# Kernel optimization log

Hardware: AMD Instinct MI355X
Metric: run time of the kernel (lower is better)

The kernel has to match this reference:

```python
import jax, jax.numpy as jnp
import numpy as np

S, B, D, H, V, MF = 50, 128, 512, 512, 30000, 32
PAD = 0


def setup_inputs() -> dict:
    key = jax.random.key(0)
    ks = jax.random.split(key, 10)
    inp = {
        "user": jax.random.normal(ks[0], (B, MF), dtype=jnp.float32),
        "item": jax.random.normal(ks[1], (B, MF), dtype=jnp.float32),
        "review_input": jax.random.randint(ks[2], (S, B), 0, V, dtype=jnp.int64),
        "review_target": jax.random.randint(ks[3], (S, B), 0, V, dtype=jnp.int64),
        # learned parameters
        "word_emb": jax.random.normal(ks[4], (V, D), dtype=jnp.float32) * 0.02,
        "W_ih": jax.random.normal(ks[5], (3 * H, D), dtype=jnp.float32) * (1.0 / np.sqrt(D)),
        "W_hh": jax.random.normal(ks[6], (3 * H, H), dtype=jnp.float32) * (1.0 / np.sqrt(H)),
        "b_ih": jnp.zeros((3 * H,), dtype=jnp.float32),
        "b_hh": jnp.zeros((3 * H,), dtype=jnp.float32),
        "W_out": jax.random.normal(ks[7], (V, H), dtype=jnp.float32) * (1.0 / np.sqrt(H)),
        "b_out": jnp.zeros((V,), dtype=jnp.float32),
    }
    return inp


def _gru_forward(review_input, word_emb, W_ih, W_hh, b_ih, b_hh, W_out, b_out, batch):
    Hdim = W_hh.shape[1]
    h0 = jnp.zeros((batch, Hdim), dtype=word_emb.dtype)  # encoder returns zeros
    x = word_emb[review_input]  # [S, B, D] embedding lookup (dropout is identity in eval)

    def step(h, x_t):
        gi = x_t @ W_ih.T + b_ih            # [B, 3H]
        gh = h @ W_hh.T + b_hh              # [B, 3H]
        i_r, i_z, i_n = jnp.split(gi, 3, axis=-1)
        h_r, h_z, h_n = jnp.split(gh, 3, axis=-1)
        r = jax.nn.sigmoid(i_r + h_r)
        z = jax.nn.sigmoid(i_z + h_z)
        n = jnp.tanh(i_n + r * h_n)
        h_new = (1.0 - z) * n + z * h
        return h_new, h_new

    _, hs = jax.lax.scan(step, h0, x)       # [S, B, H]
    logits = jnp.einsum('sbh,vh->sbv', hs, W_out) + b_out  # decode from hidden_state
    return logits.reshape(-1, W_out.shape[0])  # [S*B, V], same row order as torch.cat


def reference(user, item, review_input, review_target, word_emb, W_ih, W_hh,
              b_ih, b_hh, W_out, b_out):
    batch = user.shape[0]
    logits = _gru_forward(review_input, word_emb, W_ih, W_hh, b_ih, b_hh,
                          W_out, b_out, batch)
    targets = review_target.reshape(-1)                     # [S*B]
    logp = jax.nn.log_softmax(logits, axis=-1)
    nll = -jnp.take_along_axis(logp, targets[:, None], axis=-1)[:, 0]
    mask = (targets != PAD)
    out_loss = jnp.where(mask, nll, 0.0)                    # reduction='none', ignore_index=PAD
    denom = jnp.maximum(jnp.sum(mask.astype(logits.dtype)), 1.0)
    obj = jnp.sum(out_loss) / denom                         # mean over non-pad tokens
    return (out_loss, obj)
```

## Files before the change

kernel.cpp:

```cpp
#include <hip/hip_runtime.h>
#include <hip/hip_bf16.h>

typedef __attribute__((ext_vector_type(8))) short short8;
typedef __attribute__((ext_vector_type(4))) float floatx4;

#define S_LEN  50
#define BATCH  128
#define DIM    512
#define HID    512
#define G3     1536
#define VOCAB  30000
#define TOKENS 6400
#define NB256  118
#define NVC    472
#define NWG    (25 * NB256)

__device__ __forceinline__ float bf2f(short u) {
    union { unsigned int i; float f; } c;
    c.i = ((unsigned int)(unsigned short)u) << 16;
    return c.f;
}
__device__ __forceinline__ unsigned short f2bf(float x) {
    __hip_bfloat16 h = __float2bfloat16(x);
    unsigned short u;
    __builtin_memcpy(&u, &h, 2);
    return u;
}
__device__ __forceinline__ void gl_lds16(const void* g, void* l) {
    __builtin_amdgcn_global_load_lds(
        (const __attribute__((address_space(1))) void*)g,
        (__attribute__((address_space(3))) void*)l, 16, 0, 0);
}

__global__ void k_cvt_bf16(const float* __restrict__ src,
                           unsigned short* __restrict__ dst, int n8) {
    int g = blockIdx.x * 256 + threadIdx.x;
    if (g >= n8) return;
    const float* s = src + (size_t)g * 8;
    union { short8 v; unsigned short u[8]; } o;
#pragma unroll
    for (int i = 0; i < 8; ++i) o.u[i] = f2bf(s[i]);
    *(short8*)(dst + (size_t)g * 8) = o.v;
}

__global__ void k_gather_x(const float* __restrict__ emb, const int* __restrict__ idx,
                           unsigned short* __restrict__ X) {
    int g = blockIdx.x * 256 + threadIdx.x;
    int token = g >> 6;
    int chunk = (g & 63) << 3;
    const float* src = emb + (size_t)idx[token] * DIM + chunk;
    union { short8 v; unsigned short u[8]; } o;
#pragma unroll
    for (int i = 0; i < 8; ++i) o.u[i] = f2bf(src[i]);
    *(short8*)(X + (size_t)token * DIM + chunk) = o.v;
}

__launch_bounds__(256)
__global__ void k_gemm_gi(const unsigned short* __restrict__ X,
                          const unsigned short* __restrict__ Wih,
                          const float* __restrict__ b_ih,
                          float* __restrict__ GI) {
    __shared__ unsigned short As[64][72];
    __shared__ unsigned short Bs[64][72];
    int m0 = blockIdx.x * 64;
    int n0 = blockIdx.y * 64;
    int t = threadIdx.x;
    int w = t >> 6, lane = t & 63;
    floatx4 zero = {0.f, 0.f, 0.f, 0.f};
    floatx4 acc[4];
#pragma unroll
    for (int i = 0; i < 4; ++i) acc[i] = zero;
    int srow = t >> 2, scol = (t & 3) * 16;
    for (int k0 = 0; k0 < DIM; k0 += 64) {
        *(short8*)&As[srow][scol]     = *(const short8*)(X   + (size_t)(m0 + srow) * DIM + k0 + scol);
        *(short8*)&As[srow][scol + 8] = *(const short8*)(X   + (size_t)(m0 + srow) * DIM + k0 + scol + 8);
        *(short8*)&Bs[srow][scol]     = *(const short8*)(Wih + (size_t)(n0 + srow) * DIM + k0 + scol);
        *(short8*)&Bs[srow][scol + 8] = *(const short8*)(Wih + (size_t)(n0 + srow) * DIM + k0 + scol + 8);
        __syncthreads();
#pragma unroll
        for (int kt = 0; kt < 2; ++kt) {
            short8 a = *(const short8*)&As[w * 16 + (lane & 15)][kt * 32 + (lane >> 4) * 8];
#pragma unroll
            for (int nt = 0; nt < 4; ++nt) {
                short8 b = *(const short8*)&Bs[nt * 16 + (lane & 15)][kt * 32 + (lane >> 4) * 8];
                acc[nt] = __builtin_amdgcn_mfma_f32_16x16x32_bf16(a, b, acc[nt], 0, 0, 0);
            }
        }
        __syncthreads();
    }
#pragma unroll
    for (int nt = 0; nt < 4; ++nt)
#pragma unroll
        for (int r = 0; r < 4; ++r) {
            int row = m0 + w * 16 + (lane >> 4) * 4 + r;
            int col = n0 + nt * 16 + (lane & 15);
            GI[(size_t)row * G3 + col] = acc[nt][r] + b_ih[col];
        }
}

__launch_bounds__(64)
__global__ void k_gru_step(const float* __restrict__ GI,
                           const unsigned short* __restrict__ Whh,
                           const float* __restrict__ b_hh,
                           float* __restrict__ hf,
                           const unsigned short* __restrict__ hin,
                           unsigned short* __restrict__ hout,
                           int s) {
    int lane = threadIdx.x & 63;
    int bg = blockIdx.x & 7;
    int hs = blockIdx.x >> 3;
    int jc = hs * 16 + (lane & 15);

    const unsigned short* pa  = hin + (size_t)(bg * 16 + (lane & 15)) * HID + (lane >> 4) * 8;
    const unsigned short* pb0 = Whh + (size_t)(0 * HID + jc) * DIM + (lane >> 4) * 8;
    const unsigned short* pb1 = Whh + (size_t)(1 * HID + jc) * DIM + (lane >> 4) * 8;
    const unsigned short* pb2 = Whh + (size_t)(2 * HID + jc) * DIM + (lane >> 4) * 8;

    floatx4 acc0 = {0.f, 0.f, 0.f, 0.f};
    floatx4 acc1 = {0.f, 0.f, 0.f, 0.f};
    floatx4 acc2 = {0.f, 0.f, 0.f, 0.f};
#pragma unroll
    for (int kt = 0; kt < 16; ++kt) {
        short8 a = *(const short8*)(pa + kt * 32);
        acc0 = __builtin_amdgcn_mfma_f32_16x16x32_bf16(a, *(const short8*)(pb0 + kt * 32), acc0, 0, 0, 0);
        acc1 = __builtin_amdgcn_mfma_f32_16x16x32_bf16(a, *(const short8*)(pb1 + kt * 32), acc1, 0, 0, 0);
        acc2 = __builtin_amdgcn_mfma_f32_16x16x32_bf16(a, *(const short8*)(pb2 + kt * 32), acc2, 0, 0, 0);
    }
    float bhr = b_hh[jc], bhz = b_hh[jc + 512], bhn = b_hh[jc + 1024];
#pragma unroll
    for (int r = 0; r < 4; ++r) {
        int brow = bg * 16 + (lane >> 4) * 4 + r;
        int tok = s * BATCH + brow;
        const float* gi = GI + (size_t)tok * G3;
        float rg = 1.f / (1.f + __expf(-(gi[jc] + acc0[r] + bhr)));
        float zg = 1.f / (1.f + __expf(-(gi[jc + 512] + acc1[r] + bhz)));
        float ng = tanhf(gi[jc + 1024] + rg * (acc2[r] + bhn));
        size_t hidx = (size_t)brow * HID + jc;
        float hn = (1.f - zg) * ng + zg * hf[hidx];
        hf[hidx] = hn;
        hout[hidx] = f2bf(hn);
    }
}

__launch_bounds__(1024, 4)
__global__ void k_decode(const unsigned short* __restrict__ HS,
                         const unsigned short* __restrict__ Wout,
                         const float* __restrict__ b_out,
                         float* __restrict__ partial) {
    __shared__ unsigned short As[2][256 * 64];
    __shared__ unsigned short Bs[2][256 * 64];

    int bid = blockIdx.x;
    int xcd = bid & 7, pos = bid >> 3;
    int p = (xcd < 6 ? xcd * 369 : 2214 + (xcd - 6) * 368) + pos;
    int sgrp = p / 200;
    int rr   = p - sgrp * 200;
    int mb, nb;
    if (sgrp < 14) { mb = rr >> 3; nb = sgrp * 8 + (rr & 7); }
    else           { int q6 = rr / 6; mb = q6; nb = 112 + (rr - q6 * 6); }
    int m0 = mb * 256, n0 = nb * 256;

    int t = threadIdx.x, w = t >> 6, lane = t & 63;
    int wr = w >> 2, wc = w & 3;

    floatx4 zero = {0.f, 0.f, 0.f, 0.f};
    floatx4 acc[4][4];
#pragma unroll
    for (int mi = 0; mi < 4; ++mi)
#pragma unroll
        for (int ni = 0; ni < 4; ++ni) acc[mi][ni] = zero;

    int r8  = lane >> 3;
    int cbs = ((lane & 7) ^ r8) * 16;
    int c0 = w * 2, c1 = c0 + 1;
    int rA0 = c0 * 8 + r8, rA1 = c1 * 8 + r8;
    const char* gA0 = (const char*)(HS + (size_t)(m0 + rA0) * DIM) + cbs;
    const char* gA1 = (const char*)(HS + (size_t)(m0 + rA1) * DIM) + cbs;
    int v0 = n0 + rA0; if (v0 > VOCAB - 1) v0 = VOCAB - 1;
    int v1 = n0 + rA1; if (v1 > VOCAB - 1) v1 = VOCAB - 1;
    const char* gB0 = (const char*)(Wout + (size_t)v0 * DIM) + cbs;
    const char* gB1 = (const char*)(Wout + (size_t)v1 * DIM) + cbs;

    int roA[4][2], roB[4][2];
#pragma unroll
    for (int mi = 0; mi < 4; ++mi)
#pragma unroll
        for (int kh = 0; kh < 2; ++kh) {
            int row = wr * 64 + mi * 16 + (lane & 15);
            roA[mi][kh] = (row * 128 + kh * 64 + (lane >> 4) * 16) ^ ((row & 7) << 4);
        }
#pragma unroll
    for (int ni = 0; ni < 4; ++ni)
#pragma unroll
        for (int kh = 0; kh < 2; ++kh) {
            int row = wc * 64 + ni * 16 + (lane & 15);
            roB[ni][kh] = (row * 128 + kh * 64 + (lane >> 4) * 16) ^ ((row & 7) << 4);
        }

#define STAGE(kt, buf) do { int ko_ = (kt) * 128;                        \
        gl_lds16(gA0 + ko_, (char*)As[buf] + c0 * 1024);                 \
        gl_lds16(gA1 + ko_, (char*)As[buf] + c1 * 1024);                 \
        gl_lds16(gB0 + ko_, (char*)Bs[buf] + c0 * 1024);                 \
        gl_lds16(gB1 + ko_, (char*)Bs[buf] + c1 * 1024); } while (0)

    STAGE(0, 0);
    __builtin_amdgcn_sched_barrier(0);

    for (int kt = 0; kt < 8; ++kt) {
        int cur = kt & 1;
        if (kt < 7) {
            STAGE(kt + 1, cur ^ 1);
            __builtin_amdgcn_sched_barrier(0);
            asm volatile("s_waitcnt vmcnt(4)" ::: "memory");
        } else {
            asm volatile("s_waitcnt vmcnt(0)" ::: "memory");
        }
        __builtin_amdgcn_sched_barrier(0);
        __builtin_amdgcn_s_barrier();
        __builtin_amdgcn_sched_barrier(0);
#pragma unroll
        for (int kh = 0; kh < 2; ++kh) {
            short8 af[4], bf[4];
#pragma unroll
            for (int mi = 0; mi < 4; ++mi)
                af[mi] = *(const short8*)((const char*)As[cur] + roA[mi][kh]);
#pragma unroll
            for (int ni = 0; ni < 4; ++ni)
                bf[ni] = *(const short8*)((const char*)Bs[cur] + roB[ni][kh]);
#pragma unroll
            for (int mi = 0; mi < 4; ++mi)
#pragma unroll
                for (int ni = 0; ni < 4; ++ni)
                    acc[mi][ni] = __builtin_amdgcn_mfma_f32_16x16x32_bf16(af[mi], bf[ni], acc[mi][ni], 0, 0, 0);
        }
        __builtin_amdgcn_sched_barrier(0);
        __builtin_amdgcn_s_barrier();
        __builtin_amdgcn_sched_barrier(0);
    }
#undef STAGE

    float esum[4][4];
#pragma unroll
    for (int mi = 0; mi < 4; ++mi)
#pragma unroll
        for (int r = 0; r < 4; ++r) esum[mi][r] = 0.f;
#pragma unroll
    for (int ni = 0; ni < 4; ++ni) {
        int v = n0 + wc * 64 + ni * 16 + (lane & 15);
        bool ok = v < VOCAB;
        float bo = ok ? b_out[v] : 0.f;
#pragma unroll
        for (int mi = 0; mi < 4; ++mi)
#pragma unroll
            for (int r = 0; r < 4; ++r) {
                float logit = acc[mi][ni][r] + bo;
                esum[mi][r] += ok ? __expf(logit) : 0.f;
            }
    }
#pragma unroll
    for (int d = 1; d < 16; d <<= 1)
#pragma unroll
        for (int mi = 0; mi < 4; ++mi)
#pragma unroll
            for (int r = 0; r < 4; ++r) esum[mi][r] += __shfl_xor(esum[mi][r], d, 64);
    if ((lane & 15) == 0) {
#pragma unroll
        for (int mi = 0; mi < 4; ++mi)
#pragma unroll
            for (int r = 0; r < 4; ++r) {
                int tok = m0 + wr * 64 + mi * 16 + (lane >> 4) * 4 + r;
                partial[(size_t)tok * 512 + nb * 4 + wc] = esum[mi][r];
            }
    }
}

__global__ void k_reduce_lse(const float* __restrict__ partial, float* __restrict__ lse) {
    int tok = blockIdx.x * 4 + (threadIdx.x >> 6);
    int lane = threadIdx.x & 63;
    float s = 0.f;
    for (int j = lane; j < NVC; j += 64) s += partial[(size_t)tok * 512 + j];
#pragma unroll
    for (int d = 1; d < 64; d <<= 1) s += __shfl_xor(s, d, 64);
    if (lane == 0) lse[tok] = logf(s);
}

__global__ void k_tlogit(const unsigned short* __restrict__ HS,
                         const unsigned short* __restrict__ Wout,
                         const float* __restrict__ b_out,
                         const int* __restrict__ target,
                         float* __restrict__ tlg) {
    int tok = blockIdx.x * 4 + (threadIdx.x >> 6);
    int lane = threadIdx.x & 63;
    int tg = target[tok];
    short8 a = *(const short8*)(HS + (size_t)tok * DIM + lane * 8);
    short8 b = *(const short8*)(Wout + (size_t)tg * DIM + lane * 8);
    float s = 0.f;
#pragma unroll
    for (int i = 0; i < 8; ++i) s += bf2f(a[i]) * bf2f(b[i]);
#pragma unroll
    for (int d = 1; d < 64; d <<= 1) s += __shfl_xor(s, d, 64);
    if (lane == 0) tlg[tok] = s + b_out[tg];
}

__global__ void k_finalize(const float* __restrict__ lse, const float* __restrict__ tlg,
                           const int* __restrict__ target, float* __restrict__ out) {
    __shared__ float ssum[256];
    __shared__ float scnt[256];
    int t = threadIdx.x;
    float ls = 0.f, lc = 0.f;
    for (int i = t; i < TOKENS; i += 256) {
        int tg = target[i];
        float loss = (tg != 0) ? (lse[i] - tlg[i]) : 0.f;
        out[i] = loss;
        ls += loss;
        lc += (tg != 0) ? 1.f : 0.f;
    }
    ssum[t] = ls; scnt[t] = lc;
    __syncthreads();
    for (int d = 128; d > 0; d >>= 1) {
        if (t < d) { ssum[t] += ssum[t + d]; scnt[t] += scnt[t + d]; }
        __syncthreads();
    }
    if (t == 0) out[TOKENS] = ssum[0] / fmaxf(scnt[0], 1.f);
}

extern "C" void kernel_launch(void* const* d_in, const int* in_sizes, int n_in,
                              void* d_out, int out_size, void* d_ws, size_t ws_size,
                              hipStream_t stream) {
    const int*   review_input  = (const int*)d_in[2];
    const int*   review_target = (const int*)d_in[3];
    const float* word_emb      = (const float*)d_in[4];
    const float* W_ih          = (const float*)d_in[5];
    const float* W_hh          = (const float*)d_in[6];
    const float* b_ih          = (const float*)d_in[7];
    const float* b_hh          = (const float*)d_in[8];
    const float* W_out         = (const float*)d_in[9];
    const float* b_out         = (const float*)d_in[10];
    float* out = (float*)d_out;

    char* ws = (char*)d_ws;
    size_t off = 0;
    auto alloc = [&](size_t n) { char* p = ws + off; off += (n + 255) & ~(size_t)255; return p; };
    unsigned short* Xb    = (unsigned short*)alloc((size_t)TOKENS * DIM * 2);
    unsigned short* Wihb  = (unsigned short*)alloc((size_t)G3 * DIM * 2);
    unsigned short* Whhb  = (unsigned short*)alloc((size_t)G3 * HID * 2);
    unsigned short* Woutb = (unsigned short*)alloc((size_t)VOCAB * DIM * 2);
    unsigned short* HS    = (unsigned short*)alloc((size_t)TOKENS * HID * 2);
    unsigned short* hzero = (unsigned short*)alloc((size_t)BATCH * HID * 2);
    float* hf      = (float*)alloc((size_t)BATCH * HID * 4);
    float* GI      = (float*)alloc((size_t)TOKENS * G3 * 4);
    float* partial = (float*)alloc((size_t)TOKENS * 512 * 4);
    float* lse     = (float*)alloc((size_t)TOKENS * 4);
    float* tlg     = (float*)alloc((size_t)TOKENS * 4);
    (void)ws_size; (void)in_sizes; (void)n_in; (void)out_size;

    k_cvt_bf16<<<dim3((G3 * DIM / 8 + 255) / 256), dim3(256), 0, stream>>>(W_ih, Wihb, G3 * DIM / 8);
    k_cvt_bf16<<<dim3((G3 * HID / 8 + 255) / 256), dim3(256), 0, stream>>>(W_hh, Whhb, G3 * HID / 8);
    k_cvt_bf16<<<dim3((VOCAB * DIM / 8 + 255) / 256), dim3(256), 0, stream>>>(W_out, Woutb, VOCAB * DIM / 8);
    k_gather_x<<<dim3(TOKENS * DIM / 8 / 256), dim3(256), 0, stream>>>(word_emb, review_input, Xb);

    k_gemm_gi<<<dim3(TOKENS / 64, G3 / 64), dim3(256), 0, stream>>>(Xb, Wihb, b_ih, GI);

    hipMemsetAsync(hf, 0, (size_t)BATCH * HID * 4, stream);
    hipMemsetAsync(hzero, 0, (size_t)BATCH * HID * 2, stream);
    for (int s = 0; s < S_LEN; ++s) {
        const unsigned short* hin = s ? (HS + (size_t)(s - 1) * BATCH * HID) : hzero;
        unsigned short* hout = HS + (size_t)s * BATCH * HID;
        k_gru_step<<<dim3(256), dim3(64), 0, stream>>>(GI, Whhb, b_hh, hf, hin, hout, s);
    }

    k_decode<<<dim3(NWG), dim3(1024), 0, stream>>>(HS, Woutb, b_out, partial);
    k_reduce_lse<<<dim3(TOKENS / 4), dim3(256), 0, stream>>>(partial, lse);
    k_tlogit<<<dim3(TOKENS / 4), dim3(256), 0, stream>>>(HS, Woutb, b_out, review_target, tlg);
    k_finalize<<<dim3(1), dim3(256), 0, stream>>>(lse, tlg, review_target, out);
}
```

Measured before the change: 520.7 us.

## Run vocabulary decode GEMM in FP8 e4m3 with scaled MFMA

Quantizes W_out and the GRU hidden states to FP8 e4m3 and runs the large decode GEMM with the 16x16x128 f8f6f4 scaled MFMA instead of bf16 16x16x32, halving K-iterations and bytes loaded. The target-logit kernel also reads the FP8 copies so the gathered logit matches the log-sum-exp. It adds a conversion kernel for HS and risks accuracy loss from the 3-bit mantissa on logits over a 30000-entry softmax.

```diff
diff --git a/kernel.cpp b/kernel.cpp
--- a/kernel.cpp
+++ b/kernel.cpp
@@ -3,6 +3,8 @@
 
 typedef __attribute__((ext_vector_type(8))) short short8;
 typedef __attribute__((ext_vector_type(4))) float floatx4;
+typedef __attribute__((ext_vector_type(8))) int intx8;
+typedef __attribute__((ext_vector_type(4))) int intx4;
 
 #define S_LEN  50
 #define BATCH  128
@@ -26,6 +28,28 @@
     __builtin_memcpy(&u, &h, 2);
     return u;
 }
+__device__ __forceinline__ unsigned char f2e4m3(float x) {
+    union { float f; unsigned u; } v; v.f = x;
+    unsigned s = (v.u >> 24) & 0x80u;
+    v.u &= 0x7FFFFFFFu;
+    if (v.f >= 464.f) return (unsigned char)(s | 0x7E);
+    if (v.f < 0.015625f) {
+        int q = (int)rintf(v.f * 512.f);
+        return (unsigned char)(s | (unsigned)q);
+    }
+    unsigned lsb = (v.u >> 20) & 1u;
+    v.u += 0x7FFFFu + lsb;
+    unsigned e8 = ((v.u >> 23) & 0xFFu) - 120u;
+    unsigned m3 = (v.u >> 20) & 7u;
+    return (unsigned char)(s | (e8 << 3) | m3);
+}
+__device__ __forceinline__ float e4m32f(unsigned b) {
+    unsigned s = b & 0x80u, e = (b >> 3) & 0xFu, m = b & 7u;
+    if (e == 0) { float f = (float)m * 0.001953125f; return s ? -f : f; }
+    union { unsigned u; float f; } v;
+    v.u = (s << 24) | ((e + 120u) << 23) | (m << 20);
+    return v.f;
+}
 __device__ __forceinline__ void gl_lds16(const void* g, void* l) {
     __builtin_amdgcn_global_load_lds(
         (const __attribute__((address_space(1))) void*)g,
@@ -41,6 +65,28 @@
 #pragma unroll
     for (int i = 0; i < 8; ++i) o.u[i] = f2bf(s[i]);
     *(short8*)(dst + (size_t)g * 8) = o.v;
+}
+
+__global__ void k_cvt_fp8(const float* __restrict__ src,
+                          unsigned char* __restrict__ dst, int n16) {
+    int g = blockIdx.x * 256 + threadIdx.x;
+    if (g >= n16) return;
+    const float* s = src + (size_t)g * 16;
+    union { uint4 v; unsigned char b[16]; } o;
+#pragma unroll
+    for (int i = 0; i < 16; ++i) o.b[i] = f2e4m3(s[i]);
+    *(uint4*)(dst + (size_t)g * 16) = o.v;
+}
+
+__global__ void k_hs8(const unsigned short* __restrict__ src,
+                      unsigned char* __restrict__ dst, int n16) {
+    int g = blockIdx.x * 256 + threadIdx.x;
+    if (g >= n16) return;
+    const unsigned short* s = src + (size_t)g * 16;
+    union { uint4 v; unsigned char b[16]; } o;
+#pragma unroll
+    for (int i = 0; i < 16; ++i) o.b[i] = f2e4m3(bf2f((short)s[i]));
+    *(uint4*)(dst + (size_t)g * 16) = o.v;
 }
 
 __global__ void k_gather_x(const float* __restrict__ emb, const int* __restrict__ idx,
@@ -143,12 +189,12 @@
 }
 
 __launch_bounds__(1024, 4)
-__global__ void k_decode(const unsigned short* __restrict__ HS,
-                         const unsigned short* __restrict__ Wout,
+__global__ void k_decode(const unsigned char* __restrict__ HS8,
+                         const unsigned char* __restrict__ W8,
                          const float* __restrict__ b_out,
                          float* __restrict__ partial) {
-    __shared__ unsigned short As[2][256 * 64];
-    __shared__ unsigned short Bs[2][256 * 64];
+    __shared__ unsigned char As[2][32768];
+    __shared__ unsigned char Bs[2][32768];
 
     int bid = blockIdx.x;
     int xcd = bid & 7, pos = bid >> 3;
@@ -174,27 +220,27 @@
     int cbs = ((lane & 7) ^ r8) * 16;
     int c0 = w * 2, c1 = c0 + 1;
     int rA0 = c0 * 8 + r8, rA1 = c1 * 8 + r8;
-    const char* gA0 = (const char*)(HS + (size_t)(m0 + rA0) * DIM) + cbs;
-    const char* gA1 = (const char*)(HS + (size_t)(m0 + rA1) * DIM) + cbs;
+    const unsigned char* gA0 = HS8 + (size_t)(m0 + rA0) * DIM + cbs;
+    const unsigned char* gA1 = HS8 + (size_t)(m0 + rA1) * DIM + cbs;
     int v0 = n0 + rA0; if (v0 > VOCAB - 1) v0 = VOCAB - 1;
     int v1 = n0 + rA1; if (v1 > VOCAB - 1) v1 = VOCAB - 1;
-    const char* gB0 = (const char*)(Wout + (size_t)v0 * DIM) + cbs;
-    const char* gB1 = (const char*)(Wout + (size_t)v1 * DIM) + cbs;
+    const unsigned char* gB0 = W8 + (size_t)v0 * DIM + cbs;
+    const unsigned char* gB1 = W8 + (size_t)v1 * DIM + cbs;
 
     int roA[4][2], roB[4][2];
 #pragma unroll
     for (int mi = 0; mi < 4; ++mi)
 #pragma unroll
-        for (int kh = 0; kh < 2; ++kh) {
+        for (int h = 0; h < 2; ++h) {
             int row = wr * 64 + mi * 16 + (lane & 15);
-            roA[mi][kh] = (row * 128 + kh * 64 + (lane >> 4) * 16) ^ ((row & 7) << 4);
+            roA[mi][h] = (row * 128 + (lane >> 4) * 32 + h * 16) ^ ((row & 7) << 4);
         }
 #pragma unroll
     for (int ni = 0; ni < 4; ++ni)
 #pragma unroll
-        for (int kh = 0; kh < 2; ++kh) {
+        for (int h = 0; h < 2; ++h) {
             int row = wc * 64 + ni * 16 + (lane & 15);
-            roB[ni][kh] = (row * 128 + kh * 64 + (lane >> 4) * 16) ^ ((row & 7) << 4);
+            roB[ni][h] = (row * 128 + (lane >> 4) * 32 + h * 16) ^ ((row & 7) << 4);
         }
 
 #define STAGE(kt, buf) do { int ko_ = (kt) * 128;                        \
@@ -206,9 +252,9 @@
     STAGE(0, 0);
     __builtin_amdgcn_sched_barrier(0);
 
-    for (int kt = 0; kt < 8; ++kt) {
+    for (int kt = 0; kt < 4; ++kt) {
         int cur = kt & 1;
-        if (kt < 7) {
+        if (kt < 3) {
             STAGE(kt + 1, cur ^ 1);
             __builtin_amdgcn_sched_barrier(0);
             asm volatile("s_waitcnt vmcnt(4)" ::: "memory");
@@ -218,20 +264,22 @@
         __builtin_amdgcn_sched_barrier(0);
         __builtin_amdgcn_s_barrier();
         __builtin_amdgcn_sched_barrier(0);
-#pragma unroll
-        for (int kh = 0; kh < 2; ++kh) {
-            short8 af[4], bf[4];
-#pragma unroll
-            for (int mi = 0; mi < 4; ++mi)
-                af[mi] = *(const short8*)((const char*)As[cur] + roA[mi][kh]);
+        intx8 bf[4];
+#pragma unroll
+        for (int ni = 0; ni < 4; ++ni) {
+            intx4 lo = *(const intx4*)((const char*)Bs[cur] + roB[ni][0]);
+            intx4 hi = *(const intx4*)((const char*)Bs[cur] + roB[ni][1]);
+            bf[ni] = __builtin_shufflevector(lo, hi, 0, 1, 2, 3, 4, 5, 6, 7);
+        }
+#pragma unroll
+        for (int mi = 0; mi < 4; ++mi) {
+            intx4 lo = *(const intx4*)((const char*)As[cur] + roA[mi][0]);
+            intx4 hi = *(const intx4*)((const char*)As[cur] + roA[mi][1]);
+            intx8 af = __builtin_shufflevector(lo, hi, 0, 1, 2, 3, 4, 5, 6, 7);
 #pragma unroll
             for (int ni = 0; ni < 4; ++ni)
-                bf[ni] = *(const short8*)((const char*)Bs[cur] + roB[ni][kh]);
-#pragma unroll
-            for (int mi = 0; mi < 4; ++mi)
-#pragma unroll
-                for (int ni = 0; ni < 4; ++ni)
-                    acc[mi][ni] = __builtin_amdgcn_mfma_f32_16x16x32_bf16(af[mi], bf[ni], acc[mi][ni], 0, 0, 0);
+                acc[mi][ni] = __builtin_amdgcn_mfma_scale_f32_16x16x128_f8f6f4(
+                    af, bf[ni], acc[mi][ni], 0, 0, 0, 0x7F7F7F7F, 0, 0x7F7F7F7F);
         }
         __builtin_amdgcn_sched_barrier(0);
         __builtin_amdgcn_s_barrier();
@@ -284,19 +332,23 @@
     if (lane == 0) lse[tok] = logf(s);
 }
 
-__global__ void k_tlogit(const unsigned short* __restrict__ HS,
-                         const unsigned short* __restrict__ Wout,
+__global__ void k_tlogit(const unsigned char* __restrict__ HS8,
+                         const unsigned char* __restrict__ W8,
                          const float* __restrict__ b_out,
                          const int* __restrict__ target,
                          float* __restrict__ tlg) {
     int tok = blockIdx.x * 4 + (threadIdx.x >> 6);
     int lane = threadIdx.x & 63;
     int tg = target[tok];
-    short8 a = *(const short8*)(HS + (size_t)tok * DIM + lane * 8);
-    short8 b = *(const short8*)(Wout + (size_t)tg * DIM + lane * 8);
+    uint2 ha = *(const uint2*)(HS8 + (size_t)tok * DIM + lane * 8);
+    uint2 wa = *(const uint2*)(W8 + (size_t)tg * DIM + lane * 8);
     float s = 0.f;
 #pragma unroll
-    for (int i = 0; i < 8; ++i) s += bf2f(a[i]) * bf2f(b[i]);
+    for (int i = 0; i < 4; ++i)
+        s += e4m32f((ha.x >> (8 * i)) & 0xFF) * e4m32f((wa.x >> (8 * i)) & 0xFF);
+#pragma unroll
+    for (int i = 0; i < 4; ++i)
+        s += e4m32f((ha.y >> (8 * i)) & 0xFF) * e4m32f((wa.y >> (8 * i)) & 0xFF);
 #pragma unroll
     for (int d = 1; d < 64; d <<= 1) s += __shfl_xor(s, d, 64);
     if (lane == 0) tlg[tok] = s + b_out[tg];
@@ -344,8 +396,9 @@
     unsigned short* Xb    = (unsigned short*)alloc((size_t)TOKENS * DIM * 2);
     unsigned short* Wihb  = (unsigned short*)alloc((size_t)G3 * DIM * 2);
     unsigned short* Whhb  = (unsigned short*)alloc((size_t)G3 * HID * 2);
-    unsigned short* Woutb = (unsigned short*)alloc((size_t)VOCAB * DIM * 2);
+    unsigned char*  Wout8 = (unsigned char*)alloc((size_t)VOCAB * DIM);
     unsigned short* HS    = (unsigned short*)alloc((size_t)TOKENS * HID * 2);
+    unsigned char*  HS8   = (unsigned char*)alloc((size_t)TOKENS * HID);
     unsigned short* hzero = (unsigned short*)alloc((size_t)BATCH * HID * 2);
     float* hf      = (float*)alloc((size_t)BATCH * HID * 4);
     float* GI      = (float*)alloc((size_t)TOKENS * G3 * 4);
@@ -356,7 +409,7 @@
 
     k_cvt_bf16<<<dim3((G3 * DIM / 8 + 255) / 256), dim3(256), 0, stream>>>(W_ih, Wihb, G3 * DIM / 8);
     k_cvt_bf16<<<dim3((G3 * HID / 8 + 255) / 256), dim3(256), 0, stream>>>(W_hh, Whhb, G3 * HID / 8);
-    k_cvt_bf16<<<dim3((VOCAB * DIM / 8 + 255) / 256), dim3(256), 0, stream>>>(W_out, Woutb, VOCAB * DIM / 8);
+    k_cvt_fp8<<<dim3((VOCAB * DIM / 16 + 255) / 256), dim3(256), 0, stream>>>(W_out, Wout8, VOCAB * DIM / 16);
     k_gather_x<<<dim3(TOKENS * DIM / 8 / 256), dim3(256), 0, stream>>>(word_emb, review_input, Xb);
 
     k_gemm_gi<<<dim3(TOKENS / 64, G3 / 64), dim3(256), 0, stream>>>(Xb, Wihb, b_ih, GI);
@@ -368,9 +421,10 @@
         unsigned short* hout = HS + (size_t)s * BATCH * HID;
         k_gru_step<<<dim3(256), dim3(64), 0, stream>>>(GI, Whhb, b_hh, hf, hin, hout, s);
     }
-
-    k_decode<<<dim3(NWG), dim3(1024), 0, stream>>>(HS, Woutb, b_out, partial);
+    k_hs8<<<dim3((TOKENS * HID / 16 + 255) / 256), dim3(256), 0, stream>>>(HS, HS8, TOKENS * HID / 16);
+
+    k_decode<<<dim3(NWG), dim3(1024), 0, stream>>>(HS8, Wout8, b_out, partial);
     k_reduce_lse<<<dim3(TOKENS / 4), dim3(256), 0, stream>>>(partial, lse);
-    k_tlogit<<<dim3(TOKENS / 4), dim3(256), 0, stream>>>(HS, Woutb, b_out, review_target, tlg);
+    k_tlogit<<<dim3(TOKENS / 4), dim3(256), 0, stream>>>(HS8, Wout8, b_out, review_target, tlg);
     k_finalize<<<dim3(1), dim3(256), 0, stream>>>(lse, tlg, review_target, out);
 }
```

New measurement: 1.135 ms. 118% more time.
